# Kernel tuning notes

Hardware: AMD Instinct MI355X
Metric: run time of the kernel (lower is better)

The kernel has to match this reference:

```python
import jax, jax.numpy as jnp
import numpy as np

LAMDA = 0.1  # matches init_kwargs lamda

T_AVG = 8192
N_STEPS = 2048


def setup_inputs() -> dict:
    key = jax.random.key(0)
    k1, k2 = jax.random.split(key)
    n = N_STEPS * T_AVG
    return {
        "input": jax.random.normal(k1, (n,), dtype=jnp.float32),
        "target": jax.random.normal(k2, (n,), dtype=jnp.float32),
        "Taverage": T_AVG,
        "nSteps": N_STEPS,
    }


def reference(input, target, Taverage, nSteps):
    T = int(Taverage)
    N = int(nSteps)
    # nested loop == sum of squared diffs between consecutive length-T blocks
    x = input[: N * T].reshape(N, T)          # [N, T]
    d = x[:-1] - x[1:]                        # [N-1, T]
    sum_accum = jnp.sum(d * d)
    nom_l1 = jnp.where(N != 1, LAMDA * jnp.sqrt(sum_accum), jnp.float32(0.0))
    mse = jnp.mean((input - target) ** 2)     # MSELoss(size_average=True)
    return mse + nom_l1
```

## Files before the change

### kernel.cpp

```cpp
#include <hip/hip_runtime.h>
#include <hip/hip_bf16.h>


#define LAMDA 0.1

__global__ __launch_bounds__(256) void cyclic_reduce_kernel(
    const float4* __restrict__ in4,
    const float4* __restrict__ tg4,
    const int* __restrict__ pT,
    const int* __restrict__ pN,
    long long n,
    double* __restrict__ ws)
{
    const int T = pT[0];
    const int N = pN[0];
    const long long n4 = n >> 2;
    const long long limit = (long long)(N - 1) * (long long)T;
    const long long limit4 = limit >> 2;
    const long long t4 = (long long)T >> 2;

    float mse_acc = 0.0f;
    float dif_acc = 0.0f;

    const long long stride = (long long)gridDim.x * blockDim.x;
    for (long long i = (long long)blockIdx.x * blockDim.x + threadIdx.x;
         i < n4; i += stride) {
        float4 a = in4[i];
        float4 b = tg4[i];
        float e0 = a.x - b.x, e1 = a.y - b.y, e2 = a.z - b.z, e3 = a.w - b.w;
        mse_acc += e0 * e0 + e1 * e1 + e2 * e2 + e3 * e3;
        if (i < limit4) {
            float4 c = in4[i + t4];
            float d0 = a.x - c.x, d1 = a.y - c.y, d2 = a.z - c.z, d3 = a.w - c.w;
            dif_acc += d0 * d0 + d1 * d1 + d2 * d2 + d3 * d3;
        }
    }

    {
        const float* in = (const float*)in4;
        const float* tg = (const float*)tg4;
        long long gid = (long long)blockIdx.x * blockDim.x + threadIdx.x;
        long long tail_start = n4 << 2;
        long long idx = tail_start + gid;
        if (idx < n) {
            float e = in[idx] - tg[idx];
            mse_acc += e * e;
        }
        long long dtail_start = limit4 << 2;
        long long didx = dtail_start + gid;
        if (didx < limit) {
            float d = in[didx] - in[didx + T];
            dif_acc += d * d;
        }
    }

    #pragma unroll
    for (int off = 32; off > 0; off >>= 1) {
        mse_acc += __shfl_down(mse_acc, off, 64);
        dif_acc += __shfl_down(dif_acc, off, 64);
    }

    __shared__ float s_m[4];
    __shared__ float s_d[4];
    const int wave = threadIdx.x >> 6;
    if ((threadIdx.x & 63) == 0) {
        s_m[wave] = mse_acc;
        s_d[wave] = dif_acc;
    }
    __syncthreads();
    if (threadIdx.x == 0) {
        double m = (double)s_m[0] + (double)s_m[1] + (double)s_m[2] + (double)s_m[3];
        double d = (double)s_d[0] + (double)s_d[1] + (double)s_d[2] + (double)s_d[3];
        atomicAdd(&ws[0], m);
        atomicAdd(&ws[1], d);
    }
}

__global__ void cyclic_finalize_kernel(const double* __restrict__ ws,
                                       const int* __restrict__ pN,
                                       float* __restrict__ out,
                                       long long n)
{
    if (threadIdx.x == 0 && blockIdx.x == 0) {
        double mse = ws[0] / (double)n;
        double nom = (pN[0] != 1) ? (LAMDA * sqrt(ws[1])) : 0.0;
        out[0] = (float)(mse + nom);
    }
}

extern "C" void kernel_launch(void* const* d_in, const int* in_sizes, int n_in,
                              void* d_out, int out_size, void* d_ws, size_t ws_size,
                              hipStream_t stream) {
    const float* input  = (const float*)d_in[0];
    const float* target = (const float*)d_in[1];
    const int*   pT     = (const int*)d_in[2];
    const int*   pN     = (const int*)d_in[3];
    float* out = (float*)d_out;
    double* ws = (double*)d_ws;

    const long long n = (long long)in_sizes[0];

    hipMemsetAsync(ws, 0, 2 * sizeof(double), stream);

    const int block = 256;
    const int grid = 2048;
    cyclic_reduce_kernel<<<grid, block, 0, stream>>>(
        (const float4*)input, (const float4*)target, pT, pN, n, ws);

    cyclic_finalize_kernel<<<1, 64, 0, stream>>>(ws, pN, out, n);
}
```

Before: 181.2 us.

## Reuse input rows across a 16-row column strip and fuse finalize via last-block reduction

Each thread now walks a column through a strip of 16 consecutive rows and keeps those row values in registers. The consecutive-row difference therefore reuses loaded data instead of reading the input a second time at offset T. The separate finalize kernel is replaced by a last-block-done pattern that uses per-block partials and an atomic counter, and the grid shrinks from 2048 to 1024 blocks. This is meant to cut input traffic from roughly three streams to two plus 1/16, and to remove one kernel launch. In exchange each thread holds 17 float4 values in registers, and the memory access pattern becomes strided by row.

New measurement: 194.6 us. 7.4% more time.

```diff
diff --git a/kernel.cpp b/kernel.cpp
--- a/kernel.cpp
+++ b/kernel.cpp
@@ -1,56 +1,76 @@
 #include <hip/hip_runtime.h>
-#include <hip/hip_bf16.h>
 
 
 #define LAMDA 0.1
+#define ROWS 16
+#define BLOCK 256
 
-__global__ __launch_bounds__(256) void cyclic_reduce_kernel(
+__global__ __launch_bounds__(BLOCK) void cyclic_fused_kernel(
     const float4* __restrict__ in4,
     const float4* __restrict__ tg4,
     const int* __restrict__ pT,
     const int* __restrict__ pN,
     long long n,
-    double* __restrict__ ws)
+    double* __restrict__ m_part,
+    double* __restrict__ d_part,
+    unsigned int* __restrict__ counter,
+    float* __restrict__ out)
 {
     const int T = pT[0];
     const int N = pN[0];
-    const long long n4 = n >> 2;
-    const long long limit = (long long)(N - 1) * (long long)T;
-    const long long limit4 = limit >> 2;
     const long long t4 = (long long)T >> 2;
+    const long long segs = ((long long)N + ROWS - 1) / ROWS;
+    const long long W = t4 * segs;
 
     float mse_acc = 0.0f;
     float dif_acc = 0.0f;
 
-    const long long stride = (long long)gridDim.x * blockDim.x;
-    for (long long i = (long long)blockIdx.x * blockDim.x + threadIdx.x;
-         i < n4; i += stride) {
-        float4 a = in4[i];
-        float4 b = tg4[i];
-        float e0 = a.x - b.x, e1 = a.y - b.y, e2 = a.z - b.z, e3 = a.w - b.w;
-        mse_acc += e0 * e0 + e1 * e1 + e2 * e2 + e3 * e3;
-        if (i < limit4) {
-            float4 c = in4[i + t4];
-            float d0 = a.x - c.x, d1 = a.y - c.y, d2 = a.z - c.z, d3 = a.w - c.w;
-            dif_acc += d0 * d0 + d1 * d1 + d2 * d2 + d3 * d3;
+    const long long gtid = (long long)blockIdx.x * BLOCK + threadIdx.x;
+    const long long stride = (long long)gridDim.x * BLOCK;
+
+    for (long long w = gtid; w < W; w += stride) {
+        const long long col = w % t4;
+        const long long seg = w / t4;
+        const int r0 = (int)(seg * ROWS);
+        const float4* pin = in4 + (long long)r0 * t4 + col;
+        const float4* ptg = tg4 + (long long)r0 * t4 + col;
+
+        float4 xa[ROWS + 1];
+        #pragma unroll
+        for (int k = 0; k < ROWS; ++k) {
+            if (r0 + k < N) {
+                xa[k] = pin[(long long)k * t4];
+                float4 b = ptg[(long long)k * t4];
+                float e0 = xa[k].x - b.x, e1 = xa[k].y - b.y;
+                float e2 = xa[k].z - b.z, e3 = xa[k].w - b.w;
+                mse_acc += e0 * e0 + e1 * e1 + e2 * e2 + e3 * e3;
+            }
+        }
+        if (r0 + ROWS < N) xa[ROWS] = pin[(long long)ROWS * t4];
+
+        #pragma unroll
+        for (int k = 0; k < ROWS; ++k) {
+            if (r0 + k + 1 < N) {
+                float4 a = xa[k], c = xa[k + 1];
+                float d0 = a.x - c.x, d1 = a.y - c.y;
+                float d2 = a.z - c.z, d3 = a.w - c.w;
+                dif_acc += d0 * d0 + d1 * d1 + d2 * d2 + d3 * d3;
+            }
         }
     }
 
     {
-        const float* in = (const float*)in4;
-        const float* tg = (const float*)tg4;
-        long long gid = (long long)blockIdx.x * blockDim.x + threadIdx.x;
-        long long tail_start = n4 << 2;
-        long long idx = tail_start + gid;
-        if (idx < n) {
-            float e = in[idx] - tg[idx];
+        const long long nt4 = ((long long)N * T) >> 2;
+        const long long n4 = n >> 2;
+        for (long long i = nt4 + gtid; i < n4; i += stride) {
+            float4 a = in4[i], b = tg4[i];
+            float e0 = a.x - b.x, e1 = a.y - b.y, e2 = a.z - b.z, e3 = a.w - b.w;
+            mse_acc += e0 * e0 + e1 * e1 + e2 * e2 + e3 * e3;
+        }
+        const long long tail = (n4 << 2) + gtid;
+        if (tail < n) {
+            float e = ((const float*)in4)[tail] - ((const float*)tg4)[tail];
             mse_acc += e * e;
-        }
-        long long dtail_start = limit4 << 2;
-        long long didx = dtail_start + gid;
-        if (didx < limit) {
-            float d = in[didx] - in[didx + T];
-            dif_acc += d * d;
         }
     }
 
@@ -59,32 +79,45 @@
         mse_acc += __shfl_down(mse_acc, off, 64);
         dif_acc += __shfl_down(dif_acc, off, 64);
     }
+    __shared__ float s_m[4], s_d[4];
+    const int wave = threadIdx.x >> 6;
+    if ((threadIdx.x & 63) == 0) { s_m[wave] = mse_acc; s_d[wave] = dif_acc; }
+    __syncthreads();
 
-    __shared__ float s_m[4];
-    __shared__ float s_d[4];
-    const int wave = threadIdx.x >> 6;
-    if ((threadIdx.x & 63) == 0) {
-        s_m[wave] = mse_acc;
-        s_d[wave] = dif_acc;
-    }
-    __syncthreads();
+    __shared__ bool isLast;
     if (threadIdx.x == 0) {
         double m = (double)s_m[0] + (double)s_m[1] + (double)s_m[2] + (double)s_m[3];
         double d = (double)s_d[0] + (double)s_d[1] + (double)s_d[2] + (double)s_d[3];
-        atomicAdd(&ws[0], m);
-        atomicAdd(&ws[1], d);
+        m_part[blockIdx.x] = m;
+        d_part[blockIdx.x] = d;
+        __threadfence();
+        unsigned int old = atomicAdd(counter, 1u);
+        isLast = (old == gridDim.x - 1);
     }
-}
+    __syncthreads();
 
-__global__ void cyclic_finalize_kernel(const double* __restrict__ ws,
-                                       const int* __restrict__ pN,
-                                       float* __restrict__ out,
-                                       long long n)
-{
-    if (threadIdx.x == 0 && blockIdx.x == 0) {
-        double mse = ws[0] / (double)n;
-        double nom = (pN[0] != 1) ? (LAMDA * sqrt(ws[1])) : 0.0;
-        out[0] = (float)(mse + nom);
+    if (isLast) {
+        __threadfence();
+        double m = 0.0, d = 0.0;
+        for (int i = threadIdx.x; i < (int)gridDim.x; i += BLOCK) {
+            m += m_part[i];
+            d += d_part[i];
+        }
+        #pragma unroll
+        for (int off = 32; off > 0; off >>= 1) {
+            m += __shfl_down(m, off, 64);
+            d += __shfl_down(d, off, 64);
+        }
+        __shared__ double f_m[4], f_d[4];
+        if ((threadIdx.x & 63) == 0) { f_m[wave] = m; f_d[wave] = d; }
+        __syncthreads();
+        if (threadIdx.x == 0) {
+            double mt = f_m[0] + f_m[1] + f_m[2] + f_m[3];
+            double dt = f_d[0] + f_d[1] + f_d[2] + f_d[3];
+            double mse = mt / (double)n;
+            double nom = (N != 1) ? (LAMDA * sqrt(dt)) : 0.0;
+            out[0] = (float)(mse + nom);
+        }
     }
 }
 
@@ -96,16 +129,17 @@
     const int*   pT     = (const int*)d_in[2];
     const int*   pN     = (const int*)d_in[3];
     float* out = (float*)d_out;
-    double* ws = (double*)d_ws;
 
     const long long n = (long long)in_sizes[0];
 
-    hipMemsetAsync(ws, 0, 2 * sizeof(double), stream);
+    const int grid = 1024;
+    double* m_part = (double*)d_ws;
+    double* d_part = m_part + grid;
+    unsigned int* counter = (unsigned int*)(d_part + grid);
 
-    const int block = 256;
-    const int grid = 2048;
-    cyclic_reduce_kernel<<<grid, block, 0, stream>>>(
-        (const float4*)input, (const float4*)target, pT, pN, n, ws);
+    hipMemsetAsync(counter, 0, sizeof(unsigned int), stream);
 
-    cyclic_finalize_kernel<<<1, 64, 0, stream>>>(ws, pN, out, n);
+    cyclic_fused_kernel<<<grid, BLOCK, 0, stream>>>(
+        (const float4*)input, (const float4*)target, pT, pN, n,
+        m_part, d_part, counter, out);
 }
```
